# Performance work log

Measured on AMD Instinct MI355X. Metric: run time of the kernel, lower is better.

Reference implementation:

```python
import jax, jax.numpy as jnp
import numpy as np

N = 131072   # total atoms in flat batch
E = 262144   # total bonds (directed edges)
G = 4096     # number of molecules (graphs)
FN = 30      # atom feature dim
FE = 11      # bond feature dim
H = 256      # hidden_dim
L = 5        # num GINE layers
BN_EPS = 1e-5


def _bn(x, g, b, m, v):
    # BatchNorm1d in eval mode: affine with running stats
    return g * (x - m) * jax.lax.rsqrt(v + BN_EPS) + b


def setup_inputs() -> dict:
    key = jax.random.key(0)
    ks = jax.random.split(key, 48)
    s = 0.05  # weight scale to keep 5-layer residual stack well-conditioned
    inp = {
        'x': jax.random.normal(ks[0], (N, FN), jnp.float32),
        'edge_index': jax.random.randint(ks[1], (2, E), 0, N),
        'batch': jnp.sort(jax.random.randint(ks[2], (N,), 0, G)),
        'edge_attr': jax.random.normal(ks[3], (E, FE), jnp.float32),
        # encoders
        'enc_w': s * jax.random.normal(ks[4], (FN, H), jnp.float32),
        'enc_b': jnp.zeros((H,), jnp.float32),
        'bond_w': s * jax.random.normal(ks[5], (FE, H), jnp.float32),
        'bond_b': jnp.zeros((H,), jnp.float32),
        # per-layer GINE params (stacked over L)
        'eps': jnp.zeros((L,), jnp.float32),
        'w1': s * jax.random.normal(ks[6], (L, H, 2 * H), jnp.float32),
        'b1': jnp.zeros((L, 2 * H), jnp.float32),
        'ibn_g': 1.0 + 0.1 * jax.random.normal(ks[7], (L, 2 * H), jnp.float32),
        'ibn_b': 0.1 * jax.random.normal(ks[8], (L, 2 * H), jnp.float32),
        'ibn_m': 0.1 * jax.random.normal(ks[9], (L, 2 * H), jnp.float32),
        'ibn_v': jnp.ones((L, 2 * H), jnp.float32),
        'w2': s * jax.random.normal(ks[10], (L, 2 * H, H), jnp.float32),
        'b2': jnp.zeros((L, H), jnp.float32),
        'obn_g': 1.0 + 0.1 * jax.random.normal(ks[11], (L, H), jnp.float32),
        'obn_b': 0.1 * jax.random.normal(ks[12], (L, H), jnp.float32),
        'obn_m': 0.1 * jax.random.normal(ks[13], (L, H), jnp.float32),
        'obn_v': jnp.ones((L, H), jnp.float32),
        # classifier
        'cw1': s * jax.random.normal(ks[14], (2 * H, H), jnp.float32),
        'cb1': jnp.zeros((H,), jnp.float32),
        'c1g': 1.0 + 0.1 * jax.random.normal(ks[15], (H,), jnp.float32),
        'c1b': 0.1 * jax.random.normal(ks[16], (H,), jnp.float32),
        'c1m': 0.1 * jax.random.normal(ks[17], (H,), jnp.float32),
        'c1v': jnp.ones((H,), jnp.float32),
        'cw2': s * jax.random.normal(ks[18], (H, H // 2), jnp.float32),
        'cb2': jnp.zeros((H // 2,), jnp.float32),
        'c2g': 1.0 + 0.1 * jax.random.normal(ks[19], (H // 2,), jnp.float32),
        'c2b': 0.1 * jax.random.normal(ks[20], (H // 2,), jnp.float32),
        'c2m': 0.1 * jax.random.normal(ks[21], (H // 2,), jnp.float32),
        'c2v': jnp.ones((H // 2,), jnp.float32),
        'cw3': s * jax.random.normal(ks[22], (H // 2, 1), jnp.float32),
        'cb3': jnp.zeros((1,), jnp.float32),
    }
    return inp


def reference(x, edge_index, batch, edge_attr,
              enc_w, enc_b, bond_w, bond_b,
              eps, w1, b1, ibn_g, ibn_b, ibn_m, ibn_v,
              w2, b2, obn_g, obn_b, obn_m, obn_v,
              cw1, cb1, c1g, c1b, c1m, c1v,
              cw2, cb2, c2g, c2b, c2m, c2v,
              cw3, cb3):
    n = x.shape[0]
    src, dst = edge_index[0], edge_index[1]
    h = x @ enc_w + enc_b                      # [N, H]
    e = edge_attr @ bond_w + bond_b           # [E, H]
    for i in range(L):
        h_in = h
        # GINEConv: (1+eps)*x_i + sum_j relu(x_j + e_ji), then MLP
        msg = jax.nn.relu(h[src] + e)                          # [E, H] gather
        agg = jax.ops.segment_sum(msg, dst, num_segments=n)    # [N, H] scatter-add
        z = (1.0 + eps[i]) * h + agg
        z = jax.nn.relu(_bn(z @ w1[i] + b1[i], ibn_g[i], ibn_b[i], ibn_m[i], ibn_v[i]))
        z = z @ w2[i] + b2[i]
        # outer BN + relu (dropout is identity in eval) + residual
        h = jax.nn.relu(_bn(z, obn_g[i], obn_b[i], obn_m[i], obn_v[i])) + h_in
    # global mean + max pooling by graph id
    counts = jax.ops.segment_sum(jnp.ones((n,), h.dtype), batch, num_segments=G)
    sums = jax.ops.segment_sum(h, batch, num_segments=G)
    mean_p = sums / jnp.maximum(counts, 1.0)[:, None]
    max_p = jax.ops.segment_max(h, batch, num_segments=G)
    max_p = jnp.where(counts[:, None] > 0, max_p, 0.0)
    p = jnp.concatenate([mean_p, max_p], axis=1)               # [G, 2H]
    # classifier (eval mode: dropout off, BN uses running stats)
    q = jax.nn.relu(_bn(p @ cw1 + cb1, c1g, c1b, c1m, c1v))
    q = jax.nn.relu(_bn(q @ cw2 + cb2, c2g, c2b, c2m, c2v))
    out = q @ cw3 + cb3
    return out[:, 0]                                           # [G]
```

## Files before the change

### kernel.cpp

```cpp
#include <hip/hip_runtime.h>
#include <math.h>

#define NA 131072
#define NE 262144
#define NG 4096
#define FN 30
#define FE 11
#define H  256
#define H2 512
#define NL 5
#define BN_EPS 1e-5f
#define KP 32

typedef _Float16 f16x8 __attribute__((ext_vector_type(8)));
typedef _Float16 f16x4 __attribute__((ext_vector_type(4)));
typedef float f32x4 __attribute__((ext_vector_type(4)));

static char* g_buf = nullptr;
__attribute__((constructor)) static void _alloc_private_ws() {
    void* p = nullptr;
    if (hipMalloc(&p, (size_t)320 * 1024 * 1024) == hipSuccess) g_buf = (char*)p;
}

__global__ __launch_bounds__(256) void prep_w_all(const float* __restrict__ w, int K, int N,
                                                  _Float16* __restrict__ hT) {
    const float* wl = w + (size_t)blockIdx.z * K * N;
    _Float16* hTl = hT + (size_t)blockIdx.z * K * N;
    __shared__ float t[32][33];
    const int k0 = blockIdx.x * 32, n0 = blockIdx.y * 32;
    const int tx = threadIdx.x & 31, ty = threadIdx.x >> 5;
    #pragma unroll
    for (int i = 0; i < 4; ++i)
        t[ty + i * 8][tx] = wl[(size_t)(k0 + ty + i * 8) * N + n0 + tx];
    __syncthreads();
    #pragma unroll
    for (int i = 0; i < 4; ++i)
        hTl[(size_t)(n0 + ty + i * 8) * K + k0 + tx] = (_Float16)t[tx][ty + i * 8];
}

__global__ __launch_bounds__(256) void prep_wpad(const float* __restrict__ w, int K_IN,
                                                 _Float16* __restrict__ wT) {
    const int n = threadIdx.x;
    #pragma unroll
    for (int kk = 0; kk < KP / 8; ++kk) {
        f16x8 v;
        #pragma unroll
        for (int j = 0; j < 8; ++j) {
            const int k = kk * 8 + j;
            v[j] = (k < K_IN) ? (_Float16)w[(size_t)k * H + n] : (_Float16)0.0f;
        }
        *(f16x8*)(wT + (size_t)n * KP + kk * 8) = v;
    }
}

__global__ __launch_bounds__(256) void prep_x16(const float* __restrict__ x,
                                                _Float16* __restrict__ x16) {
    const int row = blockIdx.x * 64 + (threadIdx.x >> 2);
    const int g = threadIdx.x & 3;
    f16x8 v;
    #pragma unroll
    for (int j = 0; j < 8; ++j) {
        const int c = g * 8 + j;
        v[j] = (c < FN) ? (_Float16)x[(size_t)row * FN + c] : (_Float16)0.0f;
    }
    *(f16x8*)(x16 + (size_t)row * KP + g * 8) = v;
}

__global__ __launch_bounds__(256) void prep_ea16(const float* __restrict__ eattr,
                                                 const int2* __restrict__ se,
                                                 _Float16* __restrict__ ea16) {
    const int t = blockIdx.x * 64 + (threadIdx.x >> 2);
    const int g = threadIdx.x & 3;
    const int e = se[t].y;
    f16x8 v;
    #pragma unroll
    for (int j = 0; j < 8; ++j) {
        const int c = g * 8 + j;
        v[j] = (c < FE) ? (_Float16)eattr[(size_t)e * FE + c] : (_Float16)0.0f;
    }
    *(f16x8*)(ea16 + (size_t)t * KP + g * 8) = v;
}

__global__ __launch_bounds__(256) void count_deg(const int* __restrict__ ei,
                                                 int* __restrict__ deg) {
    const int e = blockIdx.x * 256 + threadIdx.x;
    if (e < NE) atomicAdd(&deg[ei[NE + e]], 1);
}

__global__ __launch_bounds__(1024) void scan_deg(const int* __restrict__ deg,
                                                 int* __restrict__ rowptr,
                                                 int* __restrict__ cursor) {
    __shared__ int part[1024];
    const int t = threadIdx.x;
    const int base = t * 128;
    int s = 0;
    #pragma unroll 8
    for (int i = 0; i < 128; ++i) s += deg[base + i];
    part[t] = s;
    __syncthreads();
    for (int off = 1; off < 1024; off <<= 1) {
        const int v = (t >= off) ? part[t - off] : 0;
        __syncthreads();
        part[t] += v;
        __syncthreads();
    }
    int run = (t == 0) ? 0 : part[t - 1];
    #pragma unroll 8
    for (int i = 0; i < 128; ++i) {
        rowptr[base + i] = run;
        cursor[base + i] = run;
        run += deg[base + i];
    }
    if (t == 1023) rowptr[NA] = run;
}

__global__ __launch_bounds__(256) void fill_elist(const int* __restrict__ ei,
                                                  int* __restrict__ cursor,
                                                  int2* __restrict__ se) {
    const int e = blockIdx.x * 256 + threadIdx.x;
    if (e < NE) {
        const int src = ei[e];
        const int pos = atomicAdd(&cursor[ei[NE + e]], 1);
        se[pos] = make_int2(src, e);
    }
}

__global__ __launch_bounds__(512, 4) void fused_gine_mlp(
    const _Float16* __restrict__ Hin,
    _Float16* __restrict__ Hout,
    const _Float16* __restrict__ eb,
    const int2* __restrict__ se,
    const int* __restrict__ rowptr,
    const float* __restrict__ eps, int l,
    const _Float16* __restrict__ W1T,
    const _Float16* __restrict__ W2T,
    const float* __restrict__ b1l, const float* __restrict__ ig,
    const float* __restrict__ ib, const float* __restrict__ im,
    const float* __restrict__ iv,
    const float* __restrict__ b2l, const float* __restrict__ og,
    const float* __restrict__ ob, const float* __restrict__ om,
    const float* __restrict__ ov)
{
    __shared__ f16x8 Bs[1024];
    __shared__ _Float16 Z1[64 * 512];

    const int tid = threadIdx.x;
    const int m0 = blockIdx.x * 64;
    const int lane = tid & 63, wv = tid >> 6;
    const int lrow = lane & 15, lgrp = lane >> 4;
    const int wm2 = wv >> 2, wn2 = wv & 3;
    const int kq = tid & 3;
    const int brow = tid >> 2;
    const int bsw0 = brow * 4 + (kq ^ ((brow >> 1) & 3));
    const int bsw1 = (brow + 128) * 4 + (kq ^ (((brow + 128) >> 1) & 3));

    {
        const int c = lane * 4;
        const float sc = 1.0f + eps[l];
        #pragma unroll 1
        for (int d = 0; d < 8; ++d) {
            const int row = wv * 8 + d;
            const int dst = m0 + row;
            const f16x4 hv = *(const f16x4*)(Hin + (size_t)dst * H + c);
            float4 a;
            a.x = sc * (float)hv.x; a.y = sc * (float)hv.y;
            a.z = sc * (float)hv.z; a.w = sc * (float)hv.w;
            const int lo = rowptr[dst], hi = rowptr[dst + 1];
            for (int t = lo; t < hi; ++t) {
                const int src = se[t].x;
                const f16x4 hs = *(const f16x4*)(Hin + (size_t)src * H + c);
                const f16x4 ev = *(const f16x4*)(eb + (size_t)t * H + c);
                a.x += fmaxf((float)hs.x + (float)ev.x, 0.0f);
                a.y += fmaxf((float)hs.y + (float)ev.y, 0.0f);
                a.z += fmaxf((float)hs.z + (float)ev.z, 0.0f);
                a.w += fmaxf((float)hs.w + (float)ev.w, 0.0f);
            }
            f16x4 o;
            o.x = (_Float16)a.x; o.y = (_Float16)a.y;
            o.z = (_Float16)a.z; o.w = (_Float16)a.w;
            const int slot = 32 + ((c >> 3) ^ (row & 7));
            *(f16x4*)&Z1[row * 512 + (slot << 3) + (c & 7)] = o;
        }
    }
    __syncthreads();

    const int arA = wm2 * 32 + lrow;

    f16x8 bA, bB;
    #define SLOAD_B(BASE, K0, KD) { \
        bA = *(const f16x8*)((BASE) + (size_t)brow * (KD) + (K0) + kq * 8); \
        bB = *(const f16x8*)((BASE) + (size_t)(brow + 128) * (KD) + (K0) + kq * 8); }
    #define SWRITE_B() { Bs[bsw0] = bA; Bs[bsw1] = bB; }

    const f32x4 zero4 = {0.0f, 0.0f, 0.0f, 0.0f};

    #pragma unroll 1
    for (int h = 0; h < 2; ++h) {
        const _Float16* Bb = W1T + (size_t)h * 256 * 256;
        float scl1[4], shf1[4];
        #pragma unroll
        for (int ni = 0; ni < 4; ++ni) {
            const int c = h * 256 + wn2 * 64 + ni * 16 + lrow;
            const float s = ig[c] * rsqrtf(iv[c] + BN_EPS);
            scl1[ni] = s;
            shf1[ni] = s * (b1l[c] - im[c]) + ib[c];
        }
        f32x4 acc[2][4];
        #pragma unroll
        for (int i = 0; i < 2; ++i)
            #pragma unroll
            for (int j = 0; j < 4; ++j) acc[i][j] = zero4;

        SLOAD_B(Bb, 0, 256);
        #pragma unroll 1
        for (int ks = 0; ks < 8; ++ks) {
            __syncthreads();
            SWRITE_B();
            __syncthreads();
            if (ks + 1 < 8) SLOAD_B(Bb, (ks + 1) * 32, 256);
            f16x8 af[2], bf[4];
            #pragma unroll
            for (int mi = 0; mi < 2; ++mi) {
                const int ar = arA + mi * 16;
                const int slot = 32 + ((ks * 4 + lgrp) ^ (ar & 7));
                af[mi] = *(const f16x8*)&Z1[ar * 512 + (slot << 3)];
            }
            #pragma unroll
            for (int ni = 0; ni < 4; ++ni) {
                const int br = wn2 * 64 + ni * 16 + lrow;
                bf[ni] = Bs[br * 4 + (lgrp ^ ((br >> 1) & 3))];
            }
            #pragma unroll
            for (int mi = 0; mi < 2; ++mi)
                #pragma unroll
                for (int ni = 0; ni < 4; ++ni)
                    acc[mi][ni] = __builtin_amdgcn_mfma_f32_16x16x32_f16(af[mi], bf[ni], acc[mi][ni], 0, 0, 0);
        }
        if (h == 1) __syncthreads();
        #pragma unroll
        for (int mi = 0; mi < 2; ++mi)
            #pragma unroll
            for (int j = 0; j < 4; ++j) {
                const int row = wm2 * 32 + mi * 16 + lgrp * 4 + j;
                #pragma unroll
                for (int ni = 0; ni < 4; ++ni) {
                    const int col = h * 256 + wn2 * 64 + ni * 16 + lrow;
                    const int slot = (col >> 3) ^ (row & 7);
                    Z1[row * 512 + (slot << 3) + (col & 7)] =
                        (_Float16)fmaxf(scl1[ni] * acc[mi][ni][j] + shf1[ni], 0.0f);
                }
            }
    }

    float scl2[4], shf2[4];
    #pragma unroll
    for (int ni = 0; ni < 4; ++ni) {
        const int c = wn2 * 64 + ni * 16 + lrow;
        const float s = og[c] * rsqrtf(ov[c] + BN_EPS);
        scl2[ni] = s;
        shf2[ni] = s * (b2l[c] - om[c]) + ob[c];
    }
    f32x4 acc2[2][4];
    #pragma unroll
    for (int i = 0; i < 2; ++i)
        #pragma unroll
        for (int j = 0; j < 4; ++j) acc2[i][j] = zero4;

    SLOAD_B(W2T, 0, 512);
    #pragma unroll 1
    for (int ks = 0; ks < 16; ++ks) {
        __syncthreads();
        SWRITE_B();
        __syncthreads();
        if (ks + 1 < 16) SLOAD_B(W2T, (ks + 1) * 32, 512);
        const int k0 = ks * 32;
        f16x8 af[2], bf[4];
        #pragma unroll
        for (int mi = 0; mi < 2; ++mi) {
            const int ar = arA + mi * 16;
            const int slot = ((k0 >> 3) + lgrp) ^ (ar & 7);
            af[mi] = *(const f16x8*)&Z1[ar * 512 + (slot << 3)];
        }
        #pragma unroll
        for (int ni = 0; ni < 4; ++ni) {
            const int br = wn2 * 64 + ni * 16 + lrow;
            bf[ni] = Bs[br * 4 + (lgrp ^ ((br >> 1) & 3))];
        }
        #pragma unroll
        for (int mi = 0; mi < 2; ++mi)
            #pragma unroll
            for (int ni = 0; ni < 4; ++ni)
                acc2[mi][ni] = __builtin_amdgcn_mfma_f32_16x16x32_f16(af[mi], bf[ni], acc2[mi][ni], 0, 0, 0);
    }
    #undef SLOAD_B
    #undef SWRITE_B

    #pragma unroll
    for (int mi = 0; mi < 2; ++mi)
        #pragma unroll
        for (int j = 0; j < 4; ++j) {
            const int row = m0 + wm2 * 32 + mi * 16 + lgrp * 4 + j;
            #pragma unroll
            for (int ni = 0; ni < 4; ++ni) {
                const int col = wn2 * 64 + ni * 16 + lrow;
                float v = fmaxf(scl2[ni] * acc2[mi][ni][j] + shf2[ni], 0.0f);
                v += (float)Hin[(size_t)row * H + col];
                Hout[(size_t)row * H + col] = (_Float16)v;
            }
        }
}

template <int KDIM, int EPI>
__global__ __launch_bounds__(256, 4) void gemm_f16(
    const _Float16* __restrict__ A,
    const _Float16* __restrict__ BT,
    int Ncols,
    const float* __restrict__ bias, const float* __restrict__ bng,
    const float* __restrict__ bnb, const float* __restrict__ bnm,
    const float* __restrict__ bnv,
    _Float16* __restrict__ C16, const _Float16* __restrict__ res)
{
    __shared__ f16x8 As[2][512];
    __shared__ f16x8 Bs[2][512];

    const int tid = threadIdx.x;
    const int nt = Ncols >> 7;
    const int nwg = gridDim.x, orig = blockIdx.x;
    const int q = nwg >> 3, r = nwg & 7;
    const int xcd = orig & 7, rk = orig >> 3;
    const int wg = (xcd < r ? xcd * (q + 1) : r * (q + 1) + (xcd - r) * q) + rk;
    const int m0 = (wg / nt) * 128;
    const int n0 = (wg % nt) * 128;

    const int wid = tid >> 6, lane = tid & 63;
    const int wm = wid >> 1, wn = wid & 1;
    const int lrow = lane & 15, lgrp = lane >> 4;
    const int r0s = tid >> 2;
    const int kq  = tid & 3;
    const int sw0 = kq ^ ((r0s >> 1) & 3);
    const int sw1 = kq ^ (((r0s + 64) >> 1) & 3);

    f32x4 acc[4][4];
    const f32x4 zero4 = {0.0f, 0.0f, 0.0f, 0.0f};
    #pragma unroll
    for (int i = 0; i < 4; ++i)
        #pragma unroll
        for (int j = 0; j < 4; ++j) acc[i][j] = zero4;

    f16x8 a0, a1, b0, b1;
    #define SLOAD(K0)                                                             \
        a0 = *(const f16x8*)(A  + (size_t)(m0 + r0s) * KDIM + (K0) + kq * 8);     \
        a1 = *(const f16x8*)(A  + (size_t)(m0 + r0s + 64) * KDIM + (K0) + kq * 8);\
        b0 = *(const f16x8*)(BT + (size_t)(n0 + r0s) * KDIM + (K0) + kq * 8);     \
        b1 = *(const f16x8*)(BT + (size_t)(n0 + r0s + 64) * KDIM + (K0) + kq * 8);
    #define SWRITE(CUR)                                                           \
        As[CUR][r0s * 4 + sw0] = a0;  As[CUR][(r0s + 64) * 4 + sw1] = a1;         \
        Bs[CUR][r0s * 4 + sw0] = b0;  Bs[CUR][(r0s + 64) * 4 + sw1] = b1;

    SLOAD(0);
    int cur = 0;
    for (int k0 = 0; k0 < KDIM; k0 += 32) {
        SWRITE(cur);
        __syncthreads();
        if (k0 + 32 < KDIM) { SLOAD(k0 + 32); }
        f16x8 af[4], bf[4];
        #pragma unroll
        for (int mi = 0; mi < 4; ++mi) {
            const int ar = wm * 64 + mi * 16 + lrow;
            af[mi] = As[cur][ar * 4 + (lgrp ^ ((ar >> 1) & 3))];
        }
        #pragma unroll
        for (int ni = 0; ni < 4; ++ni) {
            const int br = wn * 64 + ni * 16 + lrow;
            bf[ni] = Bs[cur][br * 4 + (lgrp ^ ((br >> 1) & 3))];
        }
        #pragma unroll
        for (int mi = 0; mi < 4; ++mi)
            #pragma unroll
            for (int ni = 0; ni < 4; ++ni)
                acc[mi][ni] = __builtin_amdgcn_mfma_f32_16x16x32_f16(af[mi], bf[ni], acc[mi][ni], 0, 0, 0);
        cur ^= 1;
    }
    #undef SLOAD
    #undef SWRITE

    float scl[4], shf[4];
    #pragma unroll
    for (int ni = 0; ni < 4; ++ni) {
        const int c = n0 + wn * 64 + ni * 16 + lrow;
        if (EPI == 2) {
            scl[ni] = 1.0f;
            shf[ni] = bias[c];
        } else {
            const float s = bng[c] * rsqrtf(bnv[c] + BN_EPS);
            scl[ni] = s;
            shf[ni] = s * (bias[c] - bnm[c]) + bnb[c];
        }
    }
    #pragma unroll
    for (int mi = 0; mi < 4; ++mi)
        #pragma unroll
        for (int j = 0; j < 4; ++j) {
            const int row = m0 + wm * 64 + mi * 16 + lgrp * 4 + j;
            #pragma unroll
            for (int ni = 0; ni < 4; ++ni) {
                const int col = n0 + wn * 64 + ni * 16 + lrow;
                float v = scl[ni] * acc[mi][ni][j] + shf[ni];
                if (EPI != 2) v = fmaxf(v, 0.0f);
                C16[(size_t)row * Ncols + col] = (_Float16)v;
            }
        }
}

__global__ __launch_bounds__(H) void pool_kernel(const _Float16* __restrict__ h16,
                                                 const int* __restrict__ batch,
                                                 _Float16* __restrict__ p16) {
    const int g = blockIdx.x;
    const int c = threadIdx.x;
    int lo, hi;
    {
        int a = 0, b = NA;
        while (a < b) { int mid = (a + b) >> 1; if (batch[mid] < g) a = mid + 1; else b = mid; }
        lo = a;
        b = NA;
        while (a < b) { int mid = (a + b) >> 1; if (batch[mid] < g + 1) a = mid + 1; else b = mid; }
        hi = a;
    }
    float sum = 0.0f, mx = -INFINITY;
    for (int n = lo; n < hi; ++n) {
        const float v = (float)h16[(size_t)n * H + c];
        sum += v;
        mx = fmaxf(mx, v);
    }
    const int cnt = hi - lo;
    const float mean = (cnt > 0) ? sum / (float)cnt : 0.0f;
    if (cnt == 0) mx = 0.0f;
    p16[(size_t)g * H2 + c] = (_Float16)mean;
    p16[(size_t)g * H2 + H + c] = (_Float16)mx;
}

__global__ __launch_bounds__(64) void final_out(const _Float16* __restrict__ q2,
                                                const float* __restrict__ w,
                                                const float* __restrict__ b,
                                                float* __restrict__ out) {
    const int g = blockIdx.x;
    const int lane = threadIdx.x;
    float acc = (float)q2[(size_t)g * 128 + lane] * w[lane]
              + (float)q2[(size_t)g * 128 + 64 + lane] * w[64 + lane];
    #pragma unroll
    for (int off = 32; off > 0; off >>= 1) acc += __shfl_down(acc, off);
    if (lane == 0) out[g] = acc + b[0];
}

extern "C" void kernel_launch(void* const* d_in, const int* in_sizes, int n_in,
                              void* d_out, int out_size, void* d_ws, size_t ws_size,
                              hipStream_t stream) {
    const float* x      = (const float*)d_in[0];
    const int*   ei     = (const int*)d_in[1];
    const int*   batch  = (const int*)d_in[2];
    const float* eattr  = (const float*)d_in[3];
    const float* enc_w  = (const float*)d_in[4];
    const float* enc_b  = (const float*)d_in[5];
    const float* bond_w = (const float*)d_in[6];
    const float* bond_b = (const float*)d_in[7];
    const float* eps    = (const float*)d_in[8];
    const float* w1     = (const float*)d_in[9];
    const float* b1     = (const float*)d_in[10];
    const float* ibn_g  = (const float*)d_in[11];
    const float* ibn_b  = (const float*)d_in[12];
    const float* ibn_m  = (const float*)d_in[13];
    const float* ibn_v  = (const float*)d_in[14];
    const float* w2     = (const float*)d_in[15];
    const float* b2     = (const float*)d_in[16];
    const float* obn_g  = (const float*)d_in[17];
    const float* obn_b  = (const float*)d_in[18];
    const float* obn_m  = (const float*)d_in[19];
    const float* obn_v  = (const float*)d_in[20];
    const float* cw1    = (const float*)d_in[21];
    const float* cb1    = (const float*)d_in[22];
    const float* c1g    = (const float*)d_in[23];
    const float* c1b    = (const float*)d_in[24];
    const float* c1m    = (const float*)d_in[25];
    const float* c1v    = (const float*)d_in[26];
    const float* cw2    = (const float*)d_in[27];
    const float* cb2    = (const float*)d_in[28];
    const float* c2g    = (const float*)d_in[29];
    const float* c2b    = (const float*)d_in[30];
    const float* c2m    = (const float*)d_in[31];
    const float* c2v    = (const float*)d_in[32];
    const float* cw3    = (const float*)d_in[33];
    const float* cb3    = (const float*)d_in[34];
    float* out = (float*)d_out;

    const size_t WTE       = (size_t)NL * H * H2;
    const size_t CW1E      = (size_t)H2 * H;
    const size_t CW2E      = (size_t)H * (H / 2);
    const size_t EWE       = (size_t)H * KP;
    const size_t BWE       = (size_t)H * KP;
    const size_t wt_bytes  = (2 * WTE + CW1E + CW2E + EWE + BWE) * 2;
    const size_t csr_words = (size_t)3 * NA + 1 + 2 * (size_t)NE + 63;
    const size_t csr_bytes = csr_words * 4;
    const size_t eb_bytes  = (size_t)NE * H * 2;
    const size_t hx_bytes  = (size_t)NA * H * 2;
    const size_t x16_bytes = (size_t)NA * KP * 2;
    const size_t ea_bytes  = (size_t)NE * KP * 2;
    const size_t need_full = wt_bytes + csr_bytes + eb_bytes + 2 * hx_bytes
                           + x16_bytes + ea_bytes;

    char* buf;
    if (ws_size >= need_full) { buf = (char*)d_ws; }
    else if (g_buf)           { buf = g_buf; }
    else                      { buf = (char*)d_ws; }

    _Float16* w1T  = (_Float16*)buf;
    _Float16* w2T  = w1T + WTE;
    _Float16* cw1T = w2T + WTE;
    _Float16* cw2T = cw1T + CW1E;
    _Float16* encT = cw2T + CW2E;
    _Float16* bndT = encT + EWE;
    int*  deg    = (int*)(buf + wt_bytes);
    int*  rowptr = deg + NA;
    int*  cursor = rowptr + NA + 1;
    int2* se     = (int2*)(cursor + NA);
    _Float16* eb  = (_Float16*)(buf + wt_bytes + csr_bytes);
    _Float16* hA  = (_Float16*)((char*)eb + eb_bytes);
    _Float16* hB  = (_Float16*)((char*)hA + hx_bytes);
    _Float16* x16  = (_Float16*)((char*)hB + hx_bytes);
    _Float16* ea16 = (_Float16*)((char*)x16 + x16_bytes);

    _Float16* p16 = hA;
    _Float16* q1  = p16 + (size_t)NG * H2;
    _Float16* q2  = q1 + (size_t)NG * H;

    prep_w_all<<<dim3(H / 32, H2 / 32, NL), 256, 0, stream>>>(w1, H, H2, w1T);
    prep_w_all<<<dim3(H2 / 32, H / 32, NL), 256, 0, stream>>>(w2, H2, H, w2T);
    prep_w_all<<<dim3(H2 / 32, H / 32, 1), 256, 0, stream>>>(cw1, H2, H, cw1T);
    prep_w_all<<<dim3(H / 32, H / 64, 1), 256, 0, stream>>>(cw2, H, H / 2, cw2T);
    prep_wpad<<<1, 256, 0, stream>>>(enc_w, FN, encT);
    prep_wpad<<<1, 256, 0, stream>>>(bond_w, FE, bndT);

    hipMemsetAsync(deg, 0, (size_t)NA * 4, stream);
    count_deg<<<NE / 256, 256, 0, stream>>>(ei, deg);
    scan_deg<<<1, 1024, 0, stream>>>(deg, rowptr, cursor);
    fill_elist<<<NE / 256, 256, 0, stream>>>(ei, cursor, se);

    prep_x16<<<NA / 64, 256, 0, stream>>>(x, x16);
    prep_ea16<<<NE / 64, 256, 0, stream>>>(eattr, se, ea16);

    gemm_f16<KP, 2><<<(NA / 128) * (H / 128), 256, 0, stream>>>(
        x16, encT, H, enc_b, nullptr, nullptr, nullptr, nullptr, hA, nullptr);
    gemm_f16<KP, 2><<<(NE / 128) * (H / 128), 256, 0, stream>>>(
        ea16, bndT, H, bond_b, nullptr, nullptr, nullptr, nullptr, eb, nullptr);

    for (int l = 0; l < NL; ++l) {
        _Float16* hin  = (l & 1) ? hB : hA;
        _Float16* hout = (l & 1) ? hA : hB;
        fused_gine_mlp<<<NA / 64, 512, 0, stream>>>(
            hin, hout, eb, se, rowptr, eps, l,
            w1T + (size_t)l * H * H2, w2T + (size_t)l * H2 * H,
            b1 + (size_t)l * H2, ibn_g + (size_t)l * H2, ibn_b + (size_t)l * H2,
            ibn_m + (size_t)l * H2, ibn_v + (size_t)l * H2,
            b2 + (size_t)l * H, obn_g + (size_t)l * H, obn_b + (size_t)l * H,
            obn_m + (size_t)l * H, obn_v + (size_t)l * H);
    }

    pool_kernel<<<NG, H, 0, stream>>>(hB, batch, p16);
    gemm_f16<H2, 0><<<(NG / 128) * (H / 128), 256, 0, stream>>>(
        p16, cw1T, H, cb1, c1g, c1b, c1m, c1v, q1, nullptr);
    gemm_f16<H, 0><<<(NG / 128) * ((H / 2) / 128), 256, 0, stream>>>(
        q1, cw2T, H / 2, cb2, c2g, c2b, c2m, c2v, q2, nullptr);
    final_out<<<NG, 64, 0, stream>>>(q2, cw3, cb3, out);
}
```

Measured before the change: 1.179 ms.

## Load GEMM weight fragments directly from global memory instead of LDS staging

Removes shared-memory staging of the weight tiles in the fused GINE MLP kernel. MFMA B fragments are now read straight from global memory (expected to be L2-resident), which eliminates two barriers per k-step. Both halves of the first GEMM are computed into separate accumulators before Z1 is overwritten, and the k loops are fully unrolled. This trades barrier and LDS traffic for more global or L2 loads and higher register pressure (16 accumulators for the first GEMM), which may cut occupancy under the 512x4 launch bounds.

Result: slower. 1.980 ms (+67.9%).

```diff
diff --git a/kernel.cpp b/kernel.cpp
--- a/kernel.cpp
+++ b/kernel.cpp
@@ -141,7 +141,6 @@
     const float* __restrict__ ob, const float* __restrict__ om,
     const float* __restrict__ ov)
 {
-    __shared__ f16x8 Bs[1024];
     __shared__ _Float16 Z1[64 * 512];
 
     const int tid = threadIdx.x;
@@ -149,10 +148,6 @@
     const int lane = tid & 63, wv = tid >> 6;
     const int lrow = lane & 15, lgrp = lane >> 4;
     const int wm2 = wv >> 2, wn2 = wv & 3;
-    const int kq = tid & 3;
-    const int brow = tid >> 2;
-    const int bsw0 = brow * 4 + (kq ^ ((brow >> 1) & 3));
-    const int bsw1 = (brow + 128) * 4 + (kq ^ (((brow + 128) >> 1) & 3));
 
     {
         const int c = lane * 4;
@@ -185,39 +180,31 @@
     __syncthreads();
 
     const int arA = wm2 * 32 + lrow;
-
-    f16x8 bA, bB;
-    #define SLOAD_B(BASE, K0, KD) { \
-        bA = *(const f16x8*)((BASE) + (size_t)brow * (KD) + (K0) + kq * 8); \
-        bB = *(const f16x8*)((BASE) + (size_t)(brow + 128) * (KD) + (K0) + kq * 8); }
-    #define SWRITE_B() { Bs[bsw0] = bA; Bs[bsw1] = bB; }
-
     const f32x4 zero4 = {0.0f, 0.0f, 0.0f, 0.0f};
 
-    #pragma unroll 1
-    for (int h = 0; h < 2; ++h) {
-        const _Float16* Bb = W1T + (size_t)h * 256 * 256;
-        float scl1[4], shf1[4];
+    float scl1[2][4], shf1[2][4];
+    #pragma unroll
+    for (int h = 0; h < 2; ++h)
         #pragma unroll
         for (int ni = 0; ni < 4; ++ni) {
             const int c = h * 256 + wn2 * 64 + ni * 16 + lrow;
             const float s = ig[c] * rsqrtf(iv[c] + BN_EPS);
-            scl1[ni] = s;
-            shf1[ni] = s * (b1l[c] - im[c]) + ib[c];
-        }
-        f32x4 acc[2][4];
+            scl1[h][ni] = s;
+            shf1[h][ni] = s * (b1l[c] - im[c]) + ib[c];
+        }
+    f32x4 acc1[2][2][4];
+    #pragma unroll
+    for (int h = 0; h < 2; ++h)
         #pragma unroll
         for (int i = 0; i < 2; ++i)
             #pragma unroll
-            for (int j = 0; j < 4; ++j) acc[i][j] = zero4;
-
-        SLOAD_B(Bb, 0, 256);
-        #pragma unroll 1
+            for (int j = 0; j < 4; ++j) acc1[h][i][j] = zero4;
+
+    #pragma unroll
+    for (int h = 0; h < 2; ++h) {
+        const _Float16* Bb = W1T + (size_t)h * 256 * 256;
+        #pragma unroll
         for (int ks = 0; ks < 8; ++ks) {
-            __syncthreads();
-            SWRITE_B();
-            __syncthreads();
-            if (ks + 1 < 8) SLOAD_B(Bb, (ks + 1) * 32, 256);
             f16x8 af[2], bf[4];
             #pragma unroll
             for (int mi = 0; mi < 2; ++mi) {
@@ -228,15 +215,18 @@
             #pragma unroll
             for (int ni = 0; ni < 4; ++ni) {
                 const int br = wn2 * 64 + ni * 16 + lrow;
-                bf[ni] = Bs[br * 4 + (lgrp ^ ((br >> 1) & 3))];
+                bf[ni] = *(const f16x8*)(Bb + (size_t)br * 256 + ks * 32 + lgrp * 8);
             }
             #pragma unroll
             for (int mi = 0; mi < 2; ++mi)
                 #pragma unroll
                 for (int ni = 0; ni < 4; ++ni)
-                    acc[mi][ni] = __builtin_amdgcn_mfma_f32_16x16x32_f16(af[mi], bf[ni], acc[mi][ni], 0, 0, 0);
-        }
-        if (h == 1) __syncthreads();
+                    acc1[h][mi][ni] = __builtin_amdgcn_mfma_f32_16x16x32_f16(af[mi], bf[ni], acc1[h][mi][ni], 0, 0, 0);
+        }
+    }
+    __syncthreads();
+    #pragma unroll
+    for (int h = 0; h < 2; ++h)
         #pragma unroll
         for (int mi = 0; mi < 2; ++mi)
             #pragma unroll
@@ -247,10 +237,10 @@
                     const int col = h * 256 + wn2 * 64 + ni * 16 + lrow;
                     const int slot = (col >> 3) ^ (row & 7);
                     Z1[row * 512 + (slot << 3) + (col & 7)] =
-                        (_Float16)fmaxf(scl1[ni] * acc[mi][ni][j] + shf1[ni], 0.0f);
+                        (_Float16)fmaxf(scl1[h][ni] * acc1[h][mi][ni][j] + shf1[h][ni], 0.0f);
                 }
             }
-    }
+    __syncthreads();
 
     float scl2[4], shf2[4];
     #pragma unroll
@@ -266,13 +256,8 @@
         #pragma unroll
         for (int j = 0; j < 4; ++j) acc2[i][j] = zero4;
 
-    SLOAD_B(W2T, 0, 512);
-    #pragma unroll 1
+    #pragma unroll
     for (int ks = 0; ks < 16; ++ks) {
-        __syncthreads();
-        SWRITE_B();
-        __syncthreads();
-        if (ks + 1 < 16) SLOAD_B(W2T, (ks + 1) * 32, 512);
         const int k0 = ks * 32;
         f16x8 af[2], bf[4];
         #pragma unroll
@@ -284,7 +269,7 @@
         #pragma unroll
         for (int ni = 0; ni < 4; ++ni) {
             const int br = wn2 * 64 + ni * 16 + lrow;
-            bf[ni] = Bs[br * 4 + (lgrp ^ ((br >> 1) & 3))];
+            bf[ni] = *(const f16x8*)(W2T + (size_t)br * 512 + k0 + lgrp * 8);
         }
         #pragma unroll
         for (int mi = 0; mi < 2; ++mi)
@@ -292,8 +277,6 @@
             for (int ni = 0; ni < 4; ++ni)
                 acc2[mi][ni] = __builtin_amdgcn_mfma_f32_16x16x32_f16(af[mi], bf[ni], acc2[mi][ni], 0, 0, 0);
     }
-    #undef SLOAD_B
-    #undef SWRITE_B
 
     #pragma unroll
     for (int mi = 0; mi < 2; ++mi)
```

## Recompute bond embeddings on the fly inside the fused GINE layer kernel

Applied to the files above, without the earlier changes.

Removes the precomputed [E,H] fp16 bond-embedding buffer and its GEMM. Each layer block now recomputes embeddings for its 64-edge chunks with MFMA from the padded edge attributes, folding the bias in through a constant-one column. The results are staged in shared memory and then gathered per destination row. This trades about 128MB of embedding reads per layer for a little extra MFMA work and more block-wide syncs, and it reuses the Z1 buffer as scratch. Aggregation is done chunk by chunk and added into Z1 in fp16, which could change rounding.

Measured after the change: 1.358 ms. 15.1% more time.

```diff
diff --git a/kernel.cpp b/kernel.cpp
--- a/kernel.cpp
+++ b/kernel.cpp
@@ -53,6 +53,23 @@
     }
 }
 
+__global__ __launch_bounds__(256) void prep_wpad_b(const float* __restrict__ w, int K_IN,
+                                                   const float* __restrict__ bias,
+                                                   _Float16* __restrict__ wT) {
+    const int n = threadIdx.x;
+    #pragma unroll
+    for (int kk = 0; kk < KP / 8; ++kk) {
+        f16x8 v;
+        #pragma unroll
+        for (int j = 0; j < 8; ++j) {
+            const int k = kk * 8 + j;
+            v[j] = (k < K_IN) ? (_Float16)w[(size_t)k * H + n]
+                 : ((k == 31) ? (_Float16)bias[n] : (_Float16)0.0f);
+        }
+        *(f16x8*)(wT + (size_t)n * KP + kk * 8) = v;
+    }
+}
+
 __global__ __launch_bounds__(256) void prep_x16(const float* __restrict__ x,
                                                 _Float16* __restrict__ x16) {
     const int row = blockIdx.x * 64 + (threadIdx.x >> 2);
@@ -76,7 +93,8 @@
     #pragma unroll
     for (int j = 0; j < 8; ++j) {
         const int c = g * 8 + j;
-        v[j] = (c < FE) ? (_Float16)eattr[(size_t)e * FE + c] : (_Float16)0.0f;
+        v[j] = (c < FE) ? (_Float16)eattr[(size_t)e * FE + c]
+             : ((c == 31) ? (_Float16)1.0f : (_Float16)0.0f);
     }
     *(f16x8*)(ea16 + (size_t)t * KP + g * 8) = v;
 }
@@ -128,7 +146,8 @@
 __global__ __launch_bounds__(512, 4) void fused_gine_mlp(
     const _Float16* __restrict__ Hin,
     _Float16* __restrict__ Hout,
-    const _Float16* __restrict__ eb,
+    const _Float16* __restrict__ EA,
+    const _Float16* __restrict__ BND,
     const int2* __restrict__ se,
     const int* __restrict__ rowptr,
     const float* __restrict__ eps, int l,
@@ -154,32 +173,99 @@
     const int bsw0 = brow * 4 + (kq ^ ((brow >> 1) & 3));
     const int bsw1 = (brow + 128) * 4 + (kq ^ (((brow + 128) >> 1) & 3));
 
+    const f32x4 zero4 = {0.0f, 0.0f, 0.0f, 0.0f};
+
     {
         const int c = lane * 4;
         const float sc = 1.0f + eps[l];
-        #pragma unroll 1
+        #pragma unroll
         for (int d = 0; d < 8; ++d) {
             const int row = wv * 8 + d;
-            const int dst = m0 + row;
-            const f16x4 hv = *(const f16x4*)(Hin + (size_t)dst * H + c);
-            float4 a;
-            a.x = sc * (float)hv.x; a.y = sc * (float)hv.y;
-            a.z = sc * (float)hv.z; a.w = sc * (float)hv.w;
-            const int lo = rowptr[dst], hi = rowptr[dst + 1];
-            for (int t = lo; t < hi; ++t) {
-                const int src = se[t].x;
-                const f16x4 hs = *(const f16x4*)(Hin + (size_t)src * H + c);
-                const f16x4 ev = *(const f16x4*)(eb + (size_t)t * H + c);
-                a.x += fmaxf((float)hs.x + (float)ev.x, 0.0f);
-                a.y += fmaxf((float)hs.y + (float)ev.y, 0.0f);
-                a.z += fmaxf((float)hs.z + (float)ev.z, 0.0f);
-                a.w += fmaxf((float)hs.w + (float)ev.w, 0.0f);
-            }
+            const f16x4 hv = *(const f16x4*)(Hin + (size_t)(m0 + row) * H + c);
             f16x4 o;
-            o.x = (_Float16)a.x; o.y = (_Float16)a.y;
-            o.z = (_Float16)a.z; o.w = (_Float16)a.w;
+            o.x = (_Float16)(sc * (float)hv.x);
+            o.y = (_Float16)(sc * (float)hv.y);
+            o.z = (_Float16)(sc * (float)hv.z);
+            o.w = (_Float16)(sc * (float)hv.w);
             const int slot = 32 + ((c >> 3) ^ (row & 7));
             *(f16x4*)&Z1[row * 512 + (slot << 3) + (c & 7)] = o;
+        }
+    }
+
+    {
+        const int elo = rowptr[m0];
+        const int ehi = rowptr[m0 + 64];
+        const int nch = (ehi - elo + 63) >> 6;
+        int tc[8], te[8];
+        #pragma unroll
+        for (int d = 0; d < 8; ++d) {
+            const int dst = m0 + wv * 8 + d;
+            tc[d] = rowptr[dst];
+            te[d] = rowptr[dst + 1];
+        }
+        const int c = lane * 4;
+        #pragma unroll 1
+        for (int ck = 0; ck < nch; ++ck) {
+            const int cb = elo + ck * 64;
+            f32x4 aeb[2][4];
+            #pragma unroll
+            for (int i = 0; i < 2; ++i)
+                #pragma unroll
+                for (int j = 0; j < 4; ++j) aeb[i][j] = zero4;
+            f16x8 af[2], bf[4];
+            #pragma unroll
+            for (int mi = 0; mi < 2; ++mi)
+                af[mi] = *(const f16x8*)(EA + (size_t)(cb + wm2 * 32 + mi * 16 + lrow) * KP + lgrp * 8);
+            #pragma unroll
+            for (int ni = 0; ni < 4; ++ni)
+                bf[ni] = *(const f16x8*)(BND + (size_t)(wn2 * 64 + ni * 16 + lrow) * KP + lgrp * 8);
+            #pragma unroll
+            for (int mi = 0; mi < 2; ++mi)
+                #pragma unroll
+                for (int ni = 0; ni < 4; ++ni)
+                    aeb[mi][ni] = __builtin_amdgcn_mfma_f32_16x16x32_f16(af[mi], bf[ni], aeb[mi][ni], 0, 0, 0);
+            __syncthreads();
+            #pragma unroll
+            for (int mi = 0; mi < 2; ++mi)
+                #pragma unroll
+                for (int j = 0; j < 4; ++j) {
+                    const int e = wm2 * 32 + mi * 16 + lgrp * 4 + j;
+                    #pragma unroll
+                    for (int ni = 0; ni < 4; ++ni) {
+                        const int col = wn2 * 64 + ni * 16 + lrow;
+                        Z1[e * 512 + col] = (_Float16)aeb[mi][ni][j];
+                    }
+                }
+            __syncthreads();
+            const int cend = cb + 64;
+            #pragma unroll
+            for (int d = 0; d < 8; ++d) {
+                if (tc[d] < te[d] && tc[d] < cend) {
+                    float4 p;
+                    p.x = 0.0f; p.y = 0.0f; p.z = 0.0f; p.w = 0.0f;
+                    do {
+                        const int t = tc[d];
+                        const int src = se[t].x;
+                        const f16x4 hs = *(const f16x4*)(Hin + (size_t)src * H + c);
+                        const f16x4 ev = *(const f16x4*)&Z1[(t - cb) * 512 + c];
+                        p.x += fmaxf((float)hs.x + (float)ev.x, 0.0f);
+                        p.y += fmaxf((float)hs.y + (float)ev.y, 0.0f);
+                        p.z += fmaxf((float)hs.z + (float)ev.z, 0.0f);
+                        p.w += fmaxf((float)hs.w + (float)ev.w, 0.0f);
+                        ++tc[d];
+                    } while (tc[d] < te[d] && tc[d] < cend);
+                    const int row = wv * 8 + d;
+                    const int slot = 32 + ((c >> 3) ^ (row & 7));
+                    _Float16* zp = &Z1[row * 512 + (slot << 3) + (c & 7)];
+                    f16x4 cur = *(f16x4*)zp;
+                    f16x4 o;
+                    o.x = (_Float16)((float)cur.x + p.x);
+                    o.y = (_Float16)((float)cur.y + p.y);
+                    o.z = (_Float16)((float)cur.z + p.z);
+                    o.w = (_Float16)((float)cur.w + p.w);
+                    *(f16x4*)zp = o;
+                }
+            }
         }
     }
     __syncthreads();
@@ -191,8 +277,6 @@
         bA = *(const f16x8*)((BASE) + (size_t)brow * (KD) + (K0) + kq * 8); \
         bB = *(const f16x8*)((BASE) + (size_t)(brow + 128) * (KD) + (K0) + kq * 8); }
     #define SWRITE_B() { Bs[bsw0] = bA; Bs[bsw1] = bB; }
-
-    const f32x4 zero4 = {0.0f, 0.0f, 0.0f, 0.0f};
 
     #pragma unroll 1
     for (int h = 0; h < 2; ++h) {
@@ -500,12 +584,10 @@
     const size_t wt_bytes  = (2 * WTE + CW1E + CW2E + EWE + BWE) * 2;
     const size_t csr_words = (size_t)3 * NA + 1 + 2 * (size_t)NE + 63;
     const size_t csr_bytes = csr_words * 4;
-    const size_t eb_bytes  = (size_t)NE * H * 2;
     const size_t hx_bytes  = (size_t)NA * H * 2;
     const size_t x16_bytes = (size_t)NA * KP * 2;
-    const size_t ea_bytes  = (size_t)NE * KP * 2;
-    const size_t need_full = wt_bytes + csr_bytes + eb_bytes + 2 * hx_bytes
-                           + x16_bytes + ea_bytes;
+    const size_t ea_bytes  = ((size_t)NE + 64) * KP * 2;
+    const size_t need_full = wt_bytes + csr_bytes + 2 * hx_bytes + x16_bytes + ea_bytes;
 
     char* buf;
     if (ws_size >= need_full) { buf = (char*)d_ws; }
@@ -522,9 +604,8 @@
     int*  rowptr = deg + NA;
     int*  cursor = rowptr + NA + 1;
     int2* se     = (int2*)(cursor + NA);
-    _Float16* eb  = (_Float16*)(buf + wt_bytes + csr_bytes);
-    _Float16* hA  = (_Float16*)((char*)eb + eb_bytes);
-    _Float16* hB  = (_Float16*)((char*)hA + hx_bytes);
+    _Float16* hA   = (_Float16*)(buf + wt_bytes + csr_bytes);
+    _Float16* hB   = (_Float16*)((char*)hA + hx_bytes);
     _Float16* x16  = (_Float16*)((char*)hB + hx_bytes);
     _Float16* ea16 = (_Float16*)((char*)x16 + x16_bytes);
 
@@ -537,7 +618,7 @@
     prep_w_all<<<dim3(H2 / 32, H / 32, 1), 256, 0, stream>>>(cw1, H2, H, cw1T);
     prep_w_all<<<dim3(H / 32, H / 64, 1), 256, 0, stream>>>(cw2, H, H / 2, cw2T);
     prep_wpad<<<1, 256, 0, stream>>>(enc_w, FN, encT);
-    prep_wpad<<<1, 256, 0, stream>>>(bond_w, FE, bndT);
+    prep_wpad_b<<<1, 256, 0, stream>>>(bond_w, FE, bond_b, bndT);
 
     hipMemsetAsync(deg, 0, (size_t)NA * 4, stream);
     count_deg<<<NE / 256, 256, 0, stream>>>(ei, deg);
@@ -549,14 +630,12 @@
 
     gemm_f16<KP, 2><<<(NA / 128) * (H / 128), 256, 0, stream>>>(
         x16, encT, H, enc_b, nullptr, nullptr, nullptr, nullptr, hA, nullptr);
-    gemm_f16<KP, 2><<<(NE / 128) * (H / 128), 256, 0, stream>>>(
-        ea16, bndT, H, bond_b, nullptr, nullptr, nullptr, nullptr, eb, nullptr);
 
     for (int l = 0; l < NL; ++l) {
         _Float16* hin  = (l & 1) ? hB : hA;
         _Float16* hout = (l & 1) ? hA : hB;
         fused_gine_mlp<<<NA / 64, 512, 0, stream>>>(
-            hin, hout, eb, se, rowptr, eps, l,
+            hin, hout, ea16, bndT, se, rowptr, eps, l,
             w1T + (size_t)l * H * H2, w2T + (size_t)l * H2 * H,
             b1 + (size_t)l * H2, ibn_g + (size_t)l * H2, ibn_b + (size_t)l * H2,
             ibn_m + (size_t)l * H2, ibn_v + (size_t)l * H2,
```
